# Optimization experiments

Measured on AMD Instinct MI355X. Metric: run time of the kernel, lower is better.

## Reference

```python
import jax, jax.numpy as jnp
import numpy as np

TOP_K = 2
N_EXPERTS = 8
N_EMBED = 1024
B, T = 4, 1024


def setup_inputs() -> dict:
    key = jax.random.key(0)
    k1, k2, k3 = jax.random.split(key, 3)
    x = jax.random.normal(k1, (B, T, N_EMBED), dtype=jnp.float32)
    wg_kernel = jax.random.normal(k2, (N_EMBED, N_EXPERTS), dtype=jnp.float32) * 0.02
    wg_bias = jnp.zeros((N_EXPERTS,), dtype=jnp.float32)
    # Experts.__call__ only uses w_c_fc: (E, C, C), stddev 0.02
    w_c_fc = jax.random.normal(k3, (N_EXPERTS, N_EMBED, N_EMBED), dtype=jnp.float32) * 0.02
    return {"x": x, "wg_kernel": wg_kernel, "wg_bias": wg_bias, "w_c_fc": w_c_fc}


def _dispatch(xb, logits, n_experts, top_k):
    # xb: (T, C), logits: (T, E)
    T, C = xb.shape
    top_k_logits, idx = jax.lax.top_k(logits, top_k)          # (T, k)
    probs = jax.nn.softmax(top_k_logits, axis=-1)             # (T, k)
    flat_idx = jnp.swapaxes(idx, 0, 1).ravel()                # (k*T,), k-major order
    one_hot = jax.nn.one_hot(flat_idx, n_experts, dtype=jnp.int32)
    pos = jnp.cumsum(one_hot, axis=0) * one_hot - 1           # running slot per expert
    pos = jnp.swapaxes(pos.reshape(top_k, T, n_experts), 0, 1).max(axis=2)  # (T, k)
    idx_tk = jnp.swapaxes(flat_idx.reshape(top_k, T), 0, 1)   # (T, k)
    cap = top_k * T
    x_rep = jnp.repeat(xb, top_k, axis=0)                     # (T*k, C), token-major
    buf = jnp.zeros((n_experts, cap, C), xb.dtype)
    buf = buf.at[idx_tk.ravel(), pos.ravel()].add(x_rep)      # scatter dispatch
    return probs, pos, idx_tk, buf


def reference(x, wg_kernel, wg_bias, w_c_fc):
    Bb, Tt, C = x.shape
    n_experts = w_c_fc.shape[0]
    logits = x @ wg_kernel + wg_bias                           # (B, T, E)
    probs, pos, idx, buf = jax.vmap(
        lambda xb, lb: _dispatch(xb, lb, n_experts, TOP_K))(x, logits)
    # buf: (B, E, cap, C). The original's reshape/swapaxes shuffle is a pure
    # permutation of the (B, cap) token axis that is exactly inverted after the
    # expert GEMM, so it is mathematically a no-op; apply the grouped GEMM directly.
    out = jnp.einsum('beti,eio->beto', buf, w_c_fc)            # per-expert matmul
    gathered = jax.vmap(lambda o, i, p: o[i, p])(out, idx, pos)  # (B, T, k, C)
    y = jnp.einsum('btkc,btk->btc', gathered, probs)
    return y, probs
```

## Files before the change

kernel.cpp:

```cpp
#include <hip/hip_runtime.h>
#include <math.h>

typedef __attribute__((ext_vector_type(8))) __bf16 bf16x8;
typedef __attribute__((ext_vector_type(4))) __bf16 bf16x4v;
typedef __attribute__((ext_vector_type(4))) float f32x4;

#define N_TOK  4096
#define C_DIM  1024
#define N_EXP  8
#define CAP    4096

#define WS_CNT    0
#define WS_ROUTE  4096
#define WS_PERM   32768
#define WS_XB     ((size_t)1 << 20)
#define WS_WT     (WS_XB + ((size_t)8 << 20))

#define GLD16(g, l)                                                        \
  __builtin_amdgcn_global_load_lds(                                        \
      (const __attribute__((address_space(1))) void*)(g),                  \
      (__attribute__((address_space(3))) void*)(l), 16, 0, 0)

__global__ __launch_bounds__(256)
void prep_kernel(const float* __restrict__ x, const float* __restrict__ wg,
                 const float* __restrict__ bias, const float* __restrict__ W,
                 __bf16* __restrict__ xb, int* __restrict__ routeE,
                 float* __restrict__ probs, __bf16* __restrict__ Wt,
                 int* __restrict__ cnt) {
  __shared__ __align__(16) char smem[32768];
  const int tid = threadIdx.x;

  if (blockIdx.x < 256) {
    float (*wgT)[C_DIM] = (float (*)[C_DIM])smem;
    if (blockIdx.x == 0 && tid < N_EXP) cnt[tid] = 0;

#pragma unroll
    for (int i = 0; i < 8; ++i) {
      const float4 v = ((const float4*)wg)[i * 256 + tid];
      const int f = (i * 256 + tid) * 4;
      const int c = f >> 3;
      const int e = f & 7;
      wgT[e][c] = v.x; wgT[e + 1][c] = v.y; wgT[e + 2][c] = v.z; wgT[e + 3][c] = v.w;
    }
    __syncthreads();

    const int lane = tid & 63;
    const int wv   = tid >> 6;

    for (int s = 0; s < 4; ++s) {
      const int t = blockIdx.x * 16 + wv * 4 + s;
      const float4* xrow = (const float4*)(x + (size_t)t * C_DIM);
      float acc[N_EXP];
#pragma unroll
      for (int e = 0; e < N_EXP; ++e) acc[e] = 0.f;

#pragma unroll
      for (int j = 0; j < 4; ++j) {
        const int c4 = j * 64 + lane;
        const float4 v = xrow[c4];
        bf16x4v bv = { (__bf16)v.x, (__bf16)v.y, (__bf16)v.z, (__bf16)v.w };
        *(bf16x4v*)(xb + (size_t)t * C_DIM + c4 * 4) = bv;
#pragma unroll
        for (int e = 0; e < N_EXP; ++e) {
          const float4 w = *(const float4*)&wgT[e][c4 * 4];
          acc[e] += v.x * w.x + v.y * w.y + v.z * w.z + v.w * w.w;
        }
      }

#pragma unroll
      for (int off = 32; off >= 1; off >>= 1) {
#pragma unroll
        for (int e = 0; e < N_EXP; ++e) acc[e] += __shfl_xor(acc[e], off, 64);
      }

      if (lane == 0) {
        float l[N_EXP];
#pragma unroll
        for (int e = 0; e < N_EXP; ++e) l[e] = acc[e] + bias[e];
        int e0 = 0;
#pragma unroll
        for (int e = 1; e < N_EXP; ++e) if (l[e] > l[e0]) e0 = e;
        int e1 = (e0 == 0) ? 1 : 0;
#pragma unroll
        for (int e = 0; e < N_EXP; ++e) if (e != e0 && l[e] > l[e1]) e1 = e;
        const float p0 = 1.f / (1.f + expf(l[e1] - l[e0]));
        probs[t * 2]     = p0;
        probs[t * 2 + 1] = 1.f - p0;
        routeE[t] = e0 | (e1 << 16);
      }
    }
  } else {
    __bf16 (*tile)[33] = (__bf16 (*)[33])smem;
    const int b  = blockIdx.x - 256;
    const int e  = b >> 10;
    const int r  = b & 1023;
    const int i0 = (r >> 5) * 32;
    const int o0 = (r & 31) * 32;
    const float* We  = W  + (size_t)e * C_DIM * C_DIM;
    __bf16*      Wte = Wt + (size_t)e * C_DIM * C_DIM;
    const int tx = tid & 31, ty = tid >> 5;
#pragma unroll
    for (int j = 0; j < 32; j += 8)
      tile[ty + j][tx] = (__bf16)We[(size_t)(i0 + ty + j) * C_DIM + o0 + tx];
    __syncthreads();
#pragma unroll
    for (int j = 0; j < 32; j += 8)
      Wte[(size_t)(o0 + ty + j) * C_DIM + i0 + tx] = tile[tx][ty + j];
  }
}

__global__ __launch_bounds__(64)
void build_perm(const int* __restrict__ routeE, int* __restrict__ cnt,
                int* __restrict__ perm) {
  __shared__ int lcnt[N_EXP], base[N_EXP];
  const int tid = threadIdx.x;
  if (tid < N_EXP) lcnt[tid] = 0;
  __syncthreads();
  const int t  = blockIdx.x * 64 + tid;
  const int re = routeE[t];
  const int e0 = re & 0xffff, e1 = re >> 16;
  const int s0 = atomicAdd(&lcnt[e0], 1);
  const int s1 = atomicAdd(&lcnt[e1], 1);
  __syncthreads();
  if (tid < N_EXP) base[tid] = atomicAdd(&cnt[tid], lcnt[tid]);
  __syncthreads();
  perm[e0 * CAP + base[e0] + s0] = t * 2;
  perm[e1 * CAP + base[e1] + s1] = t * 2 + 1;
}

__global__ __launch_bounds__(256)
void moe_gemm(const __bf16* __restrict__ xb, const __bf16* __restrict__ Wt,
              const int* __restrict__ cnt, const int* __restrict__ perm,
              __bf16* __restrict__ buf) {
  const int e  = blockIdx.z;
  const int n0 = blockIdx.x * 128;
  const int m0 = blockIdx.y * 128;
  const int count = cnt[e];
  if (m0 >= count) return;

  const int*    permE = perm + e * CAP;
  const __bf16* We    = Wt + (size_t)e * C_DIM * C_DIM;

  __shared__ char AsB[16384];
  __shared__ char BsB[16384];
  __bf16* As = (__bf16*)AsB;
  __bf16* Bs = (__bf16*)BsB;

  const int tid  = threadIdx.x;
  const int lane = tid & 63;
  const int wv   = tid >> 6;
  const int wr = wv >> 1, wc = wv & 1;
  const int mw = wr * 64, nw = wc * 64;
  const int l16 = lane & 15, quad = lane >> 4;

  const int rsub  = lane >> 3;
  const int chunk = (lane & 7) ^ rsub;
  int tk[4];
#pragma unroll
  for (int q = 0; q < 4; ++q) {
    const int i = m0 + wv * 32 + q * 8 + rsub;
    tk[q] = (i < count) ? (permE[i] >> 1) : 0;
  }
  const char* gB = (const char*)We + (size_t)(n0 + wv * 32 + rsub) * 2048 + chunk * 16;
  char* ldsA = AsB + wv * 4096;
  char* ldsB = BsB + wv * 4096;

  f32x4 acc[4][4];
  const f32x4 zero = {0.f, 0.f, 0.f, 0.f};
#pragma unroll
  for (int mi = 0; mi < 4; ++mi)
#pragma unroll
    for (int ni = 0; ni < 4; ++ni) acc[mi][ni] = zero;

  for (int kt = 0; kt < 16; ++kt) {
    const int kb = kt * 128;
#pragma unroll
    for (int q = 0; q < 4; ++q)
      GLD16((const char*)xb + (size_t)tk[q] * 2048 + kb + chunk * 16,
            ldsA + q * 1024);
#pragma unroll
    for (int q = 0; q < 4; ++q)
      GLD16(gB + (size_t)q * 8 * 2048 + kb, ldsB + q * 1024);
    __syncthreads();

#pragma unroll
    for (int ks = 0; ks < 2; ++ks) {
      bf16x8 af[4], bfr[4];
#pragma unroll
      for (int mi = 0; mi < 4; ++mi) {
        const int rA = mw + mi * 16 + l16;
        af[mi] = *(const bf16x8*)(As + rA * 64 + (((ks * 4 + quad) ^ (rA & 7)) << 3));
      }
#pragma unroll
      for (int ni = 0; ni < 4; ++ni) {
        const int rB = nw + ni * 16 + l16;
        bfr[ni] = *(const bf16x8*)(Bs + rB * 64 + (((ks * 4 + quad) ^ (rB & 7)) << 3));
      }
#pragma unroll
      for (int mi = 0; mi < 4; ++mi)
#pragma unroll
        for (int ni = 0; ni < 4; ++ni)
          acc[mi][ni] = __builtin_amdgcn_mfma_f32_16x16x32_bf16(
              af[mi], bfr[ni], acc[mi][ni], 0, 0, 0);
    }
    __syncthreads();
  }

#pragma unroll
  for (int mi = 0; mi < 4; ++mi) {
#pragma unroll
    for (int r = 0; r < 4; ++r) {
      const int i = m0 + mw + mi * 16 + quad * 4 + r;
      if (i < count) {
        const int pe = permE[i];
        __bf16* orow = buf + (size_t)(pe >> 1) * 2048 + (pe & 1) * 1024 +
                       n0 + nw + l16;
#pragma unroll
        for (int ni = 0; ni < 4; ++ni)
          orow[ni * 16] = (__bf16)acc[mi][ni][r];
      }
    }
  }
}

__global__ __launch_bounds__(256)
void combine(const float* __restrict__ probs, float* __restrict__ y) {
  const int t = blockIdx.x;
  const int c = threadIdx.x * 4;
  const __bf16* bt = (const __bf16*)(y + (size_t)t * C_DIM);
  const bf16x4v b0 = *(const bf16x4v*)(bt + c);
  const bf16x4v b1 = *(const bf16x4v*)(bt + 1024 + c);
  const float p0 = probs[2 * t], p1 = probs[2 * t + 1];
  __syncthreads();
  float4 o = { p0 * (float)b0[0] + p1 * (float)b1[0],
               p0 * (float)b0[1] + p1 * (float)b1[1],
               p0 * (float)b0[2] + p1 * (float)b1[2],
               p0 * (float)b0[3] + p1 * (float)b1[3] };
  *(float4*)(y + (size_t)t * C_DIM + c) = o;
}

extern "C" void kernel_launch(void* const* d_in, const int* in_sizes, int n_in,
                              void* d_out, int out_size, void* d_ws, size_t ws_size,
                              hipStream_t stream) {
  const float* x    = (const float*)d_in[0];
  const float* wg   = (const float*)d_in[1];
  const float* bias = (const float*)d_in[2];
  const float* wcfc = (const float*)d_in[3];

  float* y     = (float*)d_out;
  float* probs = y + (size_t)N_TOK * C_DIM;
  __bf16* buf  = (__bf16*)d_out;

  char* ws   = (char*)d_ws;
  int*    cnt    = (int*)(ws + WS_CNT);
  int*    routeE = (int*)(ws + WS_ROUTE);
  int*    perm   = (int*)(ws + WS_PERM);
  __bf16* xb     = (__bf16*)(ws + WS_XB);
  __bf16* Wt     = (__bf16*)(ws + WS_WT);

  prep_kernel<<<256 + 8192, 256, 0, stream>>>(x, wg, bias, wcfc, xb, routeE,
                                              probs, Wt, cnt);
  build_perm<<<N_TOK / 64, 64, 0, stream>>>(routeE, cnt, perm);
  moe_gemm<<<dim3(8, 32, 8), 256, 0, stream>>>(xb, Wt, cnt, perm, buf);
  combine<<<N_TOK, 256, 0, stream>>>(probs, y);
}
```

Measured before the change: 139.7 us.

## Fuse expert permutation build into prep kernel and use 32x32 MFMA tiles

The separate build_perm launch is removed. Each routing block now counts its tokens per expert in shared memory, reserves a global slot range with one atomic per expert, and writes the permutation directly, with the counter cleared by a memset before the launch. The expert GEMM switches from 16x16x32 to 32x32x16 bf16 MFMA, which needs fewer LDS fragment loads per FLOP. The cost is a memset launch in place of the kernel launch, and the epilogue store pattern changes to match the 32x32 accumulator layout.

```diff
diff --git a/kernel.cpp b/kernel.cpp
--- a/kernel.cpp
+++ b/kernel.cpp
@@ -3,7 +3,7 @@
 
 typedef __attribute__((ext_vector_type(8))) __bf16 bf16x8;
 typedef __attribute__((ext_vector_type(4))) __bf16 bf16x4v;
-typedef __attribute__((ext_vector_type(4))) float f32x4;
+typedef __attribute__((ext_vector_type(16))) float f32x16;
 
 #define N_TOK  4096
 #define C_DIM  1024
@@ -11,7 +11,6 @@
 #define CAP    4096
 
 #define WS_CNT    0
-#define WS_ROUTE  4096
 #define WS_PERM   32768
 #define WS_XB     ((size_t)1 << 20)
 #define WS_WT     (WS_XB + ((size_t)8 << 20))
@@ -24,15 +23,16 @@
 __global__ __launch_bounds__(256)
 void prep_kernel(const float* __restrict__ x, const float* __restrict__ wg,
                  const float* __restrict__ bias, const float* __restrict__ W,
-                 __bf16* __restrict__ xb, int* __restrict__ routeE,
-                 float* __restrict__ probs, __bf16* __restrict__ Wt,
-                 int* __restrict__ cnt) {
+                 __bf16* __restrict__ xb, float* __restrict__ probs,
+                 __bf16* __restrict__ Wt, int* __restrict__ cnt,
+                 int* __restrict__ perm) {
   __shared__ __align__(16) char smem[32768];
+  __shared__ int lcnt[N_EXP], base[N_EXP];
   const int tid = threadIdx.x;
 
   if (blockIdx.x < 256) {
     float (*wgT)[C_DIM] = (float (*)[C_DIM])smem;
-    if (blockIdx.x == 0 && tid < N_EXP) cnt[tid] = 0;
+    if (tid < N_EXP) lcnt[tid] = 0;
 
 #pragma unroll
     for (int i = 0; i < 8; ++i) {
@@ -46,7 +46,9 @@
 
     const int lane = tid & 63;
     const int wv   = tid >> 6;
-
+    int re0[4], re1[4], rs0[4], rs1[4];
+
+#pragma unroll
     for (int s = 0; s < 4; ++s) {
       const int t = blockIdx.x * 16 + wv * 4 + s;
       const float4* xrow = (const float4*)(x + (size_t)t * C_DIM);
@@ -86,7 +88,20 @@
         const float p0 = 1.f / (1.f + expf(l[e1] - l[e0]));
         probs[t * 2]     = p0;
         probs[t * 2 + 1] = 1.f - p0;
-        routeE[t] = e0 | (e1 << 16);
+        re0[s] = e0; re1[s] = e1;
+        rs0[s] = atomicAdd(&lcnt[e0], 1);
+        rs1[s] = atomicAdd(&lcnt[e1], 1);
+      }
+    }
+    __syncthreads();
+    if (tid < N_EXP) base[tid] = atomicAdd(&cnt[tid], lcnt[tid]);
+    __syncthreads();
+    if (lane == 0) {
+#pragma unroll
+      for (int s = 0; s < 4; ++s) {
+        const int t = blockIdx.x * 16 + wv * 4 + s;
+        perm[re0[s] * CAP + base[re0[s]] + rs0[s]] = t * 2;
+        perm[re1[s] * CAP + base[re1[s]] + rs1[s]] = t * 2 + 1;
       }
     }
   } else {
@@ -109,25 +124,6 @@
   }
 }
 
-__global__ __launch_bounds__(64)
-void build_perm(const int* __restrict__ routeE, int* __restrict__ cnt,
-                int* __restrict__ perm) {
-  __shared__ int lcnt[N_EXP], base[N_EXP];
-  const int tid = threadIdx.x;
-  if (tid < N_EXP) lcnt[tid] = 0;
-  __syncthreads();
-  const int t  = blockIdx.x * 64 + tid;
-  const int re = routeE[t];
-  const int e0 = re & 0xffff, e1 = re >> 16;
-  const int s0 = atomicAdd(&lcnt[e0], 1);
-  const int s1 = atomicAdd(&lcnt[e1], 1);
-  __syncthreads();
-  if (tid < N_EXP) base[tid] = atomicAdd(&cnt[tid], lcnt[tid]);
-  __syncthreads();
-  perm[e0 * CAP + base[e0] + s0] = t * 2;
-  perm[e1 * CAP + base[e1] + s1] = t * 2 + 1;
-}
-
 __global__ __launch_bounds__(256)
 void moe_gemm(const __bf16* __restrict__ xb, const __bf16* __restrict__ Wt,
               const int* __restrict__ cnt, const int* __restrict__ perm,
@@ -151,7 +147,7 @@
   const int wv   = tid >> 6;
   const int wr = wv >> 1, wc = wv & 1;
   const int mw = wr * 64, nw = wc * 64;
-  const int l16 = lane & 15, quad = lane >> 4;
+  const int l32 = lane & 31, hi = lane >> 5;
 
   const int rsub  = lane >> 3;
   const int chunk = (lane & 7) ^ rsub;
@@ -165,12 +161,13 @@
   char* ldsA = AsB + wv * 4096;
   char* ldsB = BsB + wv * 4096;
 
-  f32x4 acc[4][4];
-  const f32x4 zero = {0.f, 0.f, 0.f, 0.f};
-#pragma unroll
-  for (int mi = 0; mi < 4; ++mi)
-#pragma unroll
-    for (int ni = 0; ni < 4; ++ni) acc[mi][ni] = zero;
+  f32x16 acc[2][2];
+#pragma unroll
+  for (int mg = 0; mg < 2; ++mg)
+#pragma unroll
+    for (int ng = 0; ng < 2; ++ng)
+#pragma unroll
+      for (int r = 0; r < 16; ++r) acc[mg][ng][r] = 0.f;
 
   for (int kt = 0; kt < 16; ++kt) {
     const int kb = kt * 128;
@@ -184,40 +181,42 @@
     __syncthreads();
 
 #pragma unroll
-    for (int ks = 0; ks < 2; ++ks) {
-      bf16x8 af[4], bfr[4];
-#pragma unroll
-      for (int mi = 0; mi < 4; ++mi) {
-        const int rA = mw + mi * 16 + l16;
-        af[mi] = *(const bf16x8*)(As + rA * 64 + (((ks * 4 + quad) ^ (rA & 7)) << 3));
-      }
-#pragma unroll
-      for (int ni = 0; ni < 4; ++ni) {
-        const int rB = nw + ni * 16 + l16;
-        bfr[ni] = *(const bf16x8*)(Bs + rB * 64 + (((ks * 4 + quad) ^ (rB & 7)) << 3));
-      }
-#pragma unroll
-      for (int mi = 0; mi < 4; ++mi)
-#pragma unroll
-        for (int ni = 0; ni < 4; ++ni)
-          acc[mi][ni] = __builtin_amdgcn_mfma_f32_16x16x32_bf16(
-              af[mi], bfr[ni], acc[mi][ni], 0, 0, 0);
-    }
-    __syncthreads();
-  }
-
-#pragma unroll
-  for (int mi = 0; mi < 4; ++mi) {
-#pragma unroll
-    for (int r = 0; r < 4; ++r) {
-      const int i = m0 + mw + mi * 16 + quad * 4 + r;
+    for (int ks = 0; ks < 4; ++ks) {
+      const int c = ks * 2 + hi;
+      bf16x8 afr[2], bfr[2];
+#pragma unroll
+      for (int mg = 0; mg < 2; ++mg) {
+        const int rA = mw + mg * 32 + l32;
+        afr[mg] = *(const bf16x8*)(As + rA * 64 + ((c ^ (rA & 7)) << 3));
+      }
+#pragma unroll
+      for (int ng = 0; ng < 2; ++ng) {
+        const int rB = nw + ng * 32 + l32;
+        bfr[ng] = *(const bf16x8*)(Bs + rB * 64 + ((c ^ (rB & 7)) << 3));
+      }
+#pragma unroll
+      for (int mg = 0; mg < 2; ++mg)
+#pragma unroll
+        for (int ng = 0; ng < 2; ++ng)
+          acc[mg][ng] = __builtin_amdgcn_mfma_f32_32x32x16_bf16(
+              afr[mg], bfr[ng], acc[mg][ng], 0, 0, 0);
+    }
+    __syncthreads();
+  }
+
+#pragma unroll
+  for (int mg = 0; mg < 2; ++mg) {
+#pragma unroll
+    for (int r = 0; r < 16; ++r) {
+      const int row = (r & 3) + 8 * (r >> 2) + 4 * hi;
+      const int i = m0 + mw + mg * 32 + row;
       if (i < count) {
         const int pe = permE[i];
         __bf16* orow = buf + (size_t)(pe >> 1) * 2048 + (pe & 1) * 1024 +
-                       n0 + nw + l16;
-#pragma unroll
-        for (int ni = 0; ni < 4; ++ni)
-          orow[ni * 16] = (__bf16)acc[mi][ni][r];
+                       n0 + nw + l32;
+#pragma unroll
+        for (int ng = 0; ng < 2; ++ng)
+          orow[ng * 32] = (__bf16)acc[mg][ng][r];
       }
     }
   }
@@ -252,15 +251,15 @@
   __bf16* buf  = (__bf16*)d_out;
 
   char* ws   = (char*)d_ws;
-  int*    cnt    = (int*)(ws + WS_CNT);
-  int*    routeE = (int*)(ws + WS_ROUTE);
-  int*    perm   = (int*)(ws + WS_PERM);
-  __bf16* xb     = (__bf16*)(ws + WS_XB);
-  __bf16* Wt     = (__bf16*)(ws + WS_WT);
-
-  prep_kernel<<<256 + 8192, 256, 0, stream>>>(x, wg, bias, wcfc, xb, routeE,
-                                              probs, Wt, cnt);
-  build_perm<<<N_TOK / 64, 64, 0, stream>>>(routeE, cnt, perm);
+  int*    cnt  = (int*)(ws + WS_CNT);
+  int*    perm = (int*)(ws + WS_PERM);
+  __bf16* xb   = (__bf16*)(ws + WS_XB);
+  __bf16* Wt   = (__bf16*)(ws + WS_WT);
+
+  hipMemsetAsync(cnt, 0, N_EXP * sizeof(int), stream);
+
+  prep_kernel<<<256 + 8192, 256, 0, stream>>>(x, wg, bias, wcfc, xb, probs,
+                                              Wt, cnt, perm);
   moe_gemm<<<dim3(8, 32, 8), 256, 0, stream>>>(xb, Wt, cnt, perm, buf);
   combine<<<N_TOK, 256, 0, stream>>>(probs, y);
 }
```

Result: no change. 140.2 us (+0.4%).
